# Performance work log

Measured on AMD Instinct MI355X. Metric: run time of the kernel, lower is better.

The kernel has to match this reference:

```python
import jax, jax.numpy as jnp
import numpy as np
from jax import lax

IN_CH = 512
OUT_CH = 512
K = 3
W_DIM = 512
PAD = K // 2
EPS = 1e-8


def setup_inputs() -> dict:
    key = jax.random.key(0)
    k1, k2, k3, k4 = jax.random.split(key, 4)
    B, H, W = 8, 64, 64
    x = jax.random.normal(k1, (B, IN_CH, H, W), dtype=jnp.float32)
    w = jax.random.normal(k2, (B, W_DIM), dtype=jnp.float32)
    weight = jax.random.normal(k3, (OUT_CH, IN_CH, K, K), dtype=jnp.float32)
    bias = jnp.zeros((OUT_CH,), dtype=jnp.float32)
    # nn.Linear(512, in_ch): weight [in_ch, 512], bias [in_ch]
    lim = 1.0 / np.sqrt(W_DIM)
    affine_w = jax.random.uniform(k4, (IN_CH, W_DIM), dtype=jnp.float32, minval=-lim, maxval=lim)
    affine_b = jnp.zeros((IN_CH,), dtype=jnp.float32)
    return {"x": x, "w": w, "weight": weight, "bias": bias,
            "affine_w": affine_w, "affine_b": affine_b}


def _conv_one(xi, wi):
    # xi: [C, H, W], wi: [O, C, K, K] -> [O, H, W]
    out = lax.conv_general_dilated(
        xi[None], wi, window_strides=(1, 1),
        padding=[(PAD, PAD), (PAD, PAD)],
        dimension_numbers=("NCHW", "OIHW", "NCHW"))
    return out[0]


def reference(x, w, weight, bias, affine_w, affine_b):
    # style: [B, C] -> broadcast as [B, 1, C, 1, 1]
    style = w @ affine_w.T + affine_b
    wmod = weight[None] * (style[:, None, :, None, None] + 1.0)  # [B, O, C, K, K]
    # demodulate
    sigma = lax.rsqrt(jnp.sum(wmod * wmod, axis=(2, 3, 4), keepdims=True) + EPS)
    wmod = wmod * sigma
    # per-sample conv (equivalent to groups=B grouped conv)
    out = jax.vmap(_conv_one)(x, wmod)  # [B, O, H, W]
    return out + bias[None, :, None, None]
```

## Files before the change

### kernel.cpp

```cpp
#include <hip/hip_runtime.h>
#include <hip/hip_bf16.h>

typedef __attribute__((ext_vector_type(8))) short bf16x8;
typedef __attribute__((ext_vector_type(4))) float f32x4;

#define FSW(c) (((c) >> 1) & 3)

typedef __attribute__((address_space(3))) unsigned int lds_uint;
typedef const __attribute__((address_space(1))) unsigned int gl_uint;

static __device__ __forceinline__ void gll16(const ushort* g, ushort* l) {
    __builtin_amdgcn_global_load_lds((gl_uint*)g, (lds_uint*)l, 16, 0, 0);
}

static __device__ __forceinline__ uint bf16rne(float f) {
    uint u = __float_as_uint(f);
    return (u + 0x7fffu + ((u >> 16) & 1u)) >> 16;
}

__global__ void k_prep1(const float* __restrict__ weight, ushort* __restrict__ Wf,
                        float* __restrict__ wsq, const float* __restrict__ w,
                        const float* __restrict__ aw, const float* __restrict__ ab,
                        float* __restrict__ style) {
    if (blockIdx.x < 1024) {
        int t = blockIdx.x * 256 + threadIdx.x;
        int o = t >> 9, c = t & 511;
        int grp = o >> 5, rr = o & 31, fm = rr >> 4, l15r = rr & 15;
        int chunkid = c >> 5, kgw = (c >> 3) & 3, kk = c & 7;
        int lanew = kgw * 16 + l15r;
        const float* wp = weight + (size_t)t * 9;
        size_t G = (size_t)(grp * 16 + chunkid);
        size_t base = G * 9216 + (size_t)fm * 512 + (size_t)lanew * 8 + kk;
        float sq = 0.f;
        #pragma unroll
        for (int j = 0; j < 9; ++j) {
            float v = wp[j];
            sq += v * v;
            Wf[base + (size_t)j * 1024] = (ushort)bf16rne(v);
        }
        wsq[t] = sq;
    } else {
        int idx = (blockIdx.x - 1024) * 4 + (threadIdx.x >> 6);
        int lane = threadIdx.x & 63;
        int b = idx >> 9, c = idx & 511;
        const float* wp = w + b * 512;
        const float* ap = aw + (size_t)c * 512;
        float s = 0.f;
        #pragma unroll
        for (int i = 0; i < 8; ++i) s += wp[lane + i * 64] * ap[lane + i * 64];
        #pragma unroll
        for (int m = 32; m; m >>= 1) s += __shfl_xor(s, m, 64);
        if (lane == 0) style[idx] = s + ab[c] + 1.0f;
    }
}

__global__ void k_prep2(const float* __restrict__ style, const float* __restrict__ wsq,
                        float* __restrict__ sigma, const float* __restrict__ x,
                        ushort* __restrict__ xb) {
    if (blockIdx.x < 1024) {
        int idx = blockIdx.x * 4 + (threadIdx.x >> 6);
        int lane = threadIdx.x & 63;
        int b = idx >> 9, o = idx & 511;
        const float* sp = style + b * 512;
        const float* qp = wsq + (size_t)o * 512;
        float s = 0.f;
        #pragma unroll
        for (int i = 0; i < 8; ++i) {
            float st = sp[lane + i * 64];
            s += st * st * qp[lane + i * 64];
        }
        #pragma unroll
        for (int m = 32; m; m >>= 1) s += __shfl_xor(s, m, 64);
        if (lane == 0) sigma[idx] = rsqrtf(s + 1e-8f);
    } else {
        int bid = blockIdx.x - 1024;
        int b = bid >> 6, y = bid & 63;
        int xcol = threadIdx.x >> 2, cg = threadIdx.x & 3;
        const float* sp = style + b * 512;
        #pragma unroll 1
        for (int cb = 0; cb < 16; ++cb) {
            int c0 = cb * 32 + cg * 8;
            float v[8];
            #pragma unroll
            for (int j = 0; j < 8; ++j)
                v[j] = x[((size_t)(b * 512 + c0 + j) * 64 + y) * 64 + xcol] * sp[c0 + j];
            uint4 pk;
            pk.x = bf16rne(v[0]) | (bf16rne(v[1]) << 16);
            pk.y = bf16rne(v[2]) | (bf16rne(v[3]) << 16);
            pk.z = bf16rne(v[4]) | (bf16rne(v[5]) << 16);
            pk.w = bf16rne(v[6]) | (bf16rne(v[7]) << 16);
            *(uint4*)&xb[((size_t)(b * 64 + y) * 64 + xcol) * 512 + c0] = pk;
        }
    }
}

#define ALOAD(SL, DY, CC) { \
    const ushort* p_ = Wbase + (size_t)(CC) * 9216 + (DY) * 3072; \
    _Pragma("unroll") for (int q_ = 0; q_ < 6; ++q_) \
        SL[q_] = *(const uint4*)(p_ + q_ * 512); }

#define MM(AV, BV, FM, FN) \
    acc[FM][FN] = __builtin_amdgcn_mfma_f32_16x16x32_bf16( \
        *(const bf16x8*)&(AV), (BV), acc[FM][FN], 0, 0, 0)

#define HGROUP(AARR, H) \
    _Pragma("unroll") for (int dx_ = 0; dx_ < 3; ++dx_) { \
      _Pragma("unroll") for (int q_ = 0; q_ < 4; ++q_) { \
        MM(AARR[dx_ * 2 + 0], bv[dx_ * 4 + q_], 0, (H) * 4 + q_); \
        MM(AARR[dx_ * 2 + 1], bv[dx_ * 4 + q_], 1, (H) * 4 + q_); \
      } }

#define ROW(R, MFMAS) { \
    bf16x8 bv[12]; \
    _Pragma("unroll") for (int dx_ = 0; dx_ < 3; ++dx_) \
    _Pragma("unroll") for (int q_ = 0; q_ < 4; ++q_) { \
        int ci_ = dx_ + q_ * 16 + l15; \
        bv[dx_ * 4 + q_] = *(const bf16x8*)&sX[cur][((R) * 66 + ci_) * 32 + ((kg ^ FSW(ci_)) * 8)]; \
    } \
    __builtin_amdgcn_s_setprio(1); \
    MFMAS \
    __builtin_amdgcn_s_setprio(0); }

#define XSTAGE(BUF, CC) { \
    _Pragma("unroll") for (int p_ = 0; p_ < 4; ++p_) { \
        int yy_ = y0 - 1 + p_; \
        if ((unsigned)yy_ < 64u) \
            gll16(srcb + (size_t)yy_ * 32768 + (CC) * 32, \
                  &sX[BUF][(p_ * 66 + wv * 16 + 1) * 32]); \
    } }

__global__ __launch_bounds__(256, 2) void k_conv(
    const ushort* __restrict__ xb, const ushort* __restrict__ Wf,
    const float* __restrict__ sigma, const float* __restrict__ bias,
    float* __restrict__ out) {

    __shared__ ushort sX[2][4 * 66 * 32];

    const int tid = threadIdx.x, bid = blockIdx.x;
    const int ob = bid >> 8;
    const int pb = ((bid & 7) << 5) | ((bid >> 3) & 31);
    const int b = pb >> 5, y0 = (pb & 31) * 2;
    const int o0 = ob * 128;
    const int wv = tid >> 6, lane = tid & 63;
    const int l15 = lane & 15, kg = lane >> 4;

    const int scol = wv * 16 + (lane >> 2);
    const int skg = lane & 3;
    const ushort* srcb = xb + ((size_t)(b * 64) * 64 + scol) * 512
                       + (size_t)((skg ^ FSW(scol + 1)) * 8);

    const int grp = ob * 4 + wv;
    const ushort* Wbase = Wf + (size_t)grp * 147456 + lane * 8;

    f32x4 acc[2][8];
    #pragma unroll
    for (int i = 0; i < 2; ++i)
        #pragma unroll
        for (int j = 0; j < 8; ++j) acc[i][j] = (f32x4){0.f, 0.f, 0.f, 0.f};

    if (tid < 64) {
        int buf = tid >> 5, rem = tid & 31;
        int r = rem >> 3, side = (rem >> 2) & 1, sl = rem & 3;
        int cp = side * 65;
        *(uint4*)&sX[buf][(r * 66 + cp) * 32 + sl * 8] = make_uint4(0u, 0u, 0u, 0u);
    }
    if (y0 == 0 || y0 == 62) {
        const int r = (y0 == 0) ? 0 : 3;
        #pragma unroll 1
        for (int i = tid; i < 528; i += 256) {
            int buf = i >= 264, j = (i >= 264) ? i - 264 : i;
            *(uint4*)&sX[buf][(r * 66 + (j >> 2)) * 32 + (j & 3) * 8] = make_uint4(0u, 0u, 0u, 0u);
        }
    }

    XSTAGE(0, 0)
    uint4 a0[6], a1[6], a2[6];
    ALOAD(a0, 0, 0) ALOAD(a1, 1, 0) ALOAD(a2, 2, 0)
    __syncthreads();

    int cur = 0;
    #pragma unroll 1
    for (int cci = 0; cci < 16; ++cci) {
        const int ncc = (cci + 1) & 15;

        XSTAGE(cur ^ 1, ncc)

        ROW(0, HGROUP(a0, 0))
        ROW(1, HGROUP(a0, 1) HGROUP(a1, 0))
        ALOAD(a0, 0, ncc)
        ROW(2, HGROUP(a1, 1) HGROUP(a2, 0))
        ALOAD(a1, 1, ncc)
        ROW(3, HGROUP(a2, 1))

        __syncthreads();
        cur ^= 1;
        ALOAD(a2, 2, ncc)
    }

    const float* sigb = sigma + b * 512;
    #pragma unroll
    for (int fm = 0; fm < 2; ++fm) {
        #pragma unroll
        for (int j = 0; j < 4; ++j) {
            int o = o0 + wv * 32 + fm * 16 + kg * 4 + j;
            float sg = sigb[o];
            float bs = bias[o];
            float* op = out + ((size_t)(b * 512 + o) * 64 + y0) * 64;
            #pragma unroll
            for (int fn = 0; fn < 8; ++fn)
                op[(fn >> 2) * 64 + (fn & 3) * 16 + l15] = acc[fm][fn][j] * sg + bs;
        }
    }
}

extern "C" void kernel_launch(void* const* d_in, const int* in_sizes, int n_in,
                              void* d_out, int out_size, void* d_ws, size_t ws_size,
                              hipStream_t stream) {
    const float* x    = (const float*)d_in[0];
    const float* w    = (const float*)d_in[1];
    const float* wt   = (const float*)d_in[2];
    const float* bias = (const float*)d_in[3];
    const float* aw   = (const float*)d_in[4];
    const float* ab   = (const float*)d_in[5];
    float* out = (float*)d_out;

    float* style  = (float*)d_ws;
    float* sigmap = style + 4096;
    float* wsq    = sigmap + 4096;
    ushort* Wf    = (ushort*)(wsq + 512 * 512);
    ushort* xbm   = Wf + 2359296;

    k_prep1<<<2048, 256, 0, stream>>>(wt, Wf, wsq, w, aw, ab, style);
    k_prep2<<<1536, 256, 0, stream>>>(style, wsq, sigmap, x, xbm);
    k_conv <<<1024, 256, 0, stream>>>(xbm, Wf, sigmap, bias, out);
}
```

Baseline: 142.1 us.

## Use two rotating weight register buffers to allow three blocks per CU

The conv main loop now keeps two 6-entry weight-fragment register arrays instead of three. The third kernel row is loaded just before it is needed, and the loop is unrolled by two chunks so the two buffers swap roles. This frees VGPRs so launch bounds can be raised from 2 to 3 blocks per CU for more latency hiding. In exchange, the dy=2 weight load has less slack before its MFMAs, the kernel may spill under the tighter register cap, and 1024 blocks no longer divide evenly into full waves.

```diff
diff --git a/kernel.cpp b/kernel.cpp
--- a/kernel.cpp
+++ b/kernel.cpp
@@ -129,7 +129,20 @@
                   &sX[BUF][(p_ * 66 + wv * 16 + 1) * 32]); \
     } }
 
-__global__ __launch_bounds__(256, 2) void k_conv(
+#define CHUNK(CCI, NCC, A0_, A1_) { \
+    XSTAGE(cur ^ 1, NCC) \
+    ROW(0, HGROUP(A0_, 0)) \
+    ROW(1, HGROUP(A0_, 1) HGROUP(A1_, 0)) \
+    ALOAD(A0_, 2, CCI)             \
+    ROW(2, HGROUP(A1_, 1) HGROUP(A0_, 0)) \
+    ALOAD(A1_, 0, NCC)             \
+    ROW(3, HGROUP(A0_, 1)) \
+    __syncthreads(); \
+    cur ^= 1; \
+    ALOAD(A0_, 1, NCC)             \
+}
+
+__global__ __launch_bounds__(256, 3) void k_conv(
     const ushort* __restrict__ xb, const ushort* __restrict__ Wf,
     const float* __restrict__ sigma, const float* __restrict__ bias,
     float* __restrict__ out) {
@@ -174,27 +187,16 @@
     }
 
     XSTAGE(0, 0)
-    uint4 a0[6], a1[6], a2[6];
-    ALOAD(a0, 0, 0) ALOAD(a1, 1, 0) ALOAD(a2, 2, 0)
+    uint4 aX[6], aY[6];
+    ALOAD(aX, 0, 0) ALOAD(aY, 1, 0)
     __syncthreads();
 
     int cur = 0;
     #pragma unroll 1
-    for (int cci = 0; cci < 16; ++cci) {
-        const int ncc = (cci + 1) & 15;
-
-        XSTAGE(cur ^ 1, ncc)
-
-        ROW(0, HGROUP(a0, 0))
-        ROW(1, HGROUP(a0, 1) HGROUP(a1, 0))
-        ALOAD(a0, 0, ncc)
-        ROW(2, HGROUP(a1, 1) HGROUP(a2, 0))
-        ALOAD(a1, 1, ncc)
-        ROW(3, HGROUP(a2, 1))
-
-        __syncthreads();
-        cur ^= 1;
-        ALOAD(a2, 2, ncc)
+    for (int it = 0; it < 8; ++it) {
+        const int c0 = it * 2, c1 = it * 2 + 1, c2 = (it * 2 + 2) & 15;
+        CHUNK(c0, c1, aX, aY)
+        CHUNK(c1, c2, aY, aX)
     }
 
     const float* sigb = sigma + b * 512;
```

Measured after the change: 159.1 us. +12.0%, slower.
